# Kernel tuning notes

Measured on AMD Instinct MI355X. Metric: run time of the kernel, lower is better.

## Reference

```python
import jax, jax.numpy as jnp
import numpy as np

N_NODES = 50000


def gcn_conv(x, W, b, src, dst, n_nodes):
    # GCNConv (PyG defaults): h = x @ W; symmetric normalization with self-loops;
    # out[i] = sum_{(j->i) in E} d_j^-1/2 d_i^-1/2 h[j] + d_i^-1 h[i] + b
    h = x @ W
    ones = jnp.ones(src.shape[0], dtype=x.dtype)
    deg = jax.ops.segment_sum(ones, dst, num_segments=n_nodes) + 1.0  # +1 self-loop
    dinv = jax.lax.rsqrt(deg)
    norm = dinv[src] * dinv[dst]                       # [E]
    msg = h[src] * norm[:, None]                        # [E, D] gather
    agg = jax.ops.segment_sum(msg, dst, num_segments=n_nodes)  # scatter-add
    agg = agg + h * (dinv * dinv)[:, None]              # self-loop term
    return agg + b


def setup_inputs() -> dict:
    key = jax.random.key(0)
    k = jax.random.split(key, 8)
    in_dim, hid, out_dim = 128, 128, 64
    x = jax.random.normal(k[0], (N_NODES, in_dim), dtype=jnp.float32)
    edge_index = jax.random.randint(k[1], (2, 600000), 0, N_NODES, dtype=jnp.int64)
    s = 1.0 / np.sqrt(in_dim)
    W1 = jax.random.uniform(k[2], (in_dim, hid), jnp.float32, -s, s)
    b1 = jnp.zeros((hid,), jnp.float32)
    W2 = jax.random.uniform(k[3], (hid, hid), jnp.float32, -s, s)
    b2 = jnp.zeros((hid,), jnp.float32)
    W3 = jax.random.uniform(k[4], (hid, out_dim), jnp.float32, -s, s)
    b3 = jnp.zeros((out_dim,), jnp.float32)
    return {"x": x, "W1": W1, "b1": b1, "W2": W2, "b2": b2,
            "W3": W3, "b3": b3, "edge_index": edge_index}


def reference(x, W1, b1, W2, b2, W3, b3, edge_index):
    src, dst = edge_index[0], edge_index[1]
    n = x.shape[0]
    h = gcn_conv(x, W1, b1, src, dst, n)
    h = jax.nn.relu(h)  # dropout: inference-mode identity
    h = gcn_conv(h, W2, b2, src, dst, n)
    h = jax.nn.relu(h)
    h = gcn_conv(h, W3, b3, src, dst, n)
    return jax.nn.log_softmax(h, axis=-1)
```

## Files before the change

kernel.cpp:

```cpp
#include <hip/hip_runtime.h>
#include <math.h>

#define N_IN  128
#define N_HID 128
#define N_OUT 64

typedef _Float16 f16x8 __attribute__((ext_vector_type(8)));
typedef _Float16 f16x4 __attribute__((ext_vector_type(4)));
typedef float f32x4 __attribute__((ext_vector_type(4)));

__global__ void k_zero_int(int* __restrict__ p, int n) {
  int i = blockIdx.x * blockDim.x + threadIdx.x;
  if (i < n) p[i] = 0;
}

__global__ void k_hist(const int* __restrict__ dst, int E, int* __restrict__ cnt) {
  int i0 = (blockIdx.x * blockDim.x + threadIdx.x) * 4;
  int stride = gridDim.x * blockDim.x * 4;
  for (; i0 + 4 <= E; i0 += stride) {
    int4 d = *reinterpret_cast<const int4*>(&dst[i0]);
    atomicAdd(&cnt[d.x], 1);
    atomicAdd(&cnt[d.y], 1);
    atomicAdd(&cnt[d.z], 1);
    atomicAdd(&cnt[d.w], 1);
  }
  if (i0 < E)
    for (; i0 < E; ++i0) atomicAdd(&cnt[dst[i0]], 1);
}

#define SCAN_CHUNK 512

__global__ __launch_bounds__(SCAN_CHUNK) void k_block_sums(
    const int* __restrict__ cnt, int n, int* __restrict__ bsum) {
  __shared__ int s[SCAN_CHUNK];
  int i = blockIdx.x * SCAN_CHUNK + threadIdx.x;
  s[threadIdx.x] = (i < n) ? cnt[i] : 0;
  __syncthreads();
  for (int off = SCAN_CHUNK / 2; off > 0; off >>= 1) {
    if (threadIdx.x < off) s[threadIdx.x] += s[threadIdx.x + off];
    __syncthreads();
  }
  if (threadIdx.x == 0) bsum[blockIdx.x] = s[0];
}

__global__ __launch_bounds__(128) void k_scan_bsums(int* __restrict__ bsum, int nb) {
  __shared__ int s[128];
  int t = threadIdx.x;
  if (nb <= 128) {
    int v = (t < nb) ? bsum[t] : 0;
    s[t] = v;
    __syncthreads();
    for (int off = 1; off < 128; off <<= 1) {
      int u = (t >= off) ? s[t - off] : 0;
      __syncthreads();
      s[t] += u;
      __syncthreads();
    }
    if (t < nb) bsum[t] = s[t] - v;
  } else if (t == 0) {
    int acc = 0;
    for (int i = 0; i < nb; ++i) { int v = bsum[i]; bsum[i] = acc; acc += v; }
  }
}

__global__ __launch_bounds__(SCAN_CHUNK) void k_scan_final(
    const int* __restrict__ cnt, int n, const int* __restrict__ bsum,
    int* __restrict__ rowptr, float* __restrict__ dinv, int E) {
  __shared__ int s[SCAN_CHUNK];
  int i = blockIdx.x * SCAN_CHUNK + threadIdx.x;
  int v = (i < n) ? cnt[i] : 0;
  s[threadIdx.x] = v;
  __syncthreads();
  for (int off = 1; off < SCAN_CHUNK; off <<= 1) {
    int t = (threadIdx.x >= off) ? s[threadIdx.x - off] : 0;
    __syncthreads();
    s[threadIdx.x] += t;
    __syncthreads();
  }
  if (i < n) {
    rowptr[i] = bsum[blockIdx.x] + s[threadIdx.x] - v;
    dinv[i] = rsqrtf((float)v + 1.0f);
    if (i == n - 1) rowptr[n] = E;
  }
}

__global__ void k_fill(const int* __restrict__ src, const int* __restrict__ dst, int E,
                       const int* __restrict__ rowptr, int* __restrict__ cnt,
                       int* __restrict__ csr) {
  int i0 = (blockIdx.x * blockDim.x + threadIdx.x) * 4;
  int stride = gridDim.x * blockDim.x * 4;
  for (; i0 + 4 <= E; i0 += stride) {
    int4 d = *reinterpret_cast<const int4*>(&dst[i0]);
    int4 sr = *reinterpret_cast<const int4*>(&src[i0]);
    csr[rowptr[d.x] + atomicSub(&cnt[d.x], 1) - 1] = sr.x;
    csr[rowptr[d.y] + atomicSub(&cnt[d.y], 1) - 1] = sr.y;
    csr[rowptr[d.z] + atomicSub(&cnt[d.z], 1) - 1] = sr.z;
    csr[rowptr[d.w] + atomicSub(&cnt[d.w], 1) - 1] = sr.w;
  }
  if (i0 < E)
    for (; i0 < E; ++i0) {
      int d = dst[i0];
      csr[rowptr[d] + atomicSub(&cnt[d], 1) - 1] = src[i0];
    }
}

__device__ inline void pack_one(const float* __restrict__ W, _Float16* __restrict__ Wp,
                                int N, int K, int idx) {
  int l = idx & 63;
  int ts = idx >> 6;
  int KS = K / 32;
  int t = ts / KS, s = ts - t * KS;
  int col = t * 16 + (l & 15);
  int k0 = s * 32 + (l >> 4) * 8;
  f16x8 f;
#pragma unroll
  for (int j = 0; j < 8; ++j) f[j] = (_Float16)W[(size_t)(k0 + j) * N + col];
  *reinterpret_cast<f16x8*>(&Wp[(size_t)idx * 8]) = f;
}

__global__ void k_pack_all(const float* __restrict__ W1, const float* __restrict__ W2,
                           const float* __restrict__ W3, _Float16* __restrict__ Wp1,
                           _Float16* __restrict__ Wp2, _Float16* __restrict__ Wp3) {
  int idx = blockIdx.x * blockDim.x + threadIdx.x;
  if (idx < 2048) pack_one(W1, Wp1, N_HID, N_IN, idx);
  else if (idx < 4096) pack_one(W2, Wp2, N_HID, N_HID, idx - 2048);
  else if (idx < 5120) pack_one(W3, Wp3, N_OUT, N_HID, idx - 4096);
}

__global__ __launch_bounds__(256) void k_gemm1(
    const float* __restrict__ A, const _Float16* __restrict__ Wp,
    const float* __restrict__ dinv, _Float16* __restrict__ out, int M) {
  constexpr int N = N_HID, K = 128, KS = K / 32, NT = N / 16;
  int lane = threadIdx.x & 63;
  int wave = threadIdx.x >> 6;
  int rowbase = blockIdx.x * 64 + wave * 16;
  int arow = rowbase + (lane & 15);
  int arc = arow < M ? arow : M - 1;
  int k0 = (lane >> 4) * 8;

  f16x8 afrag[KS];
#pragma unroll
  for (int s = 0; s < KS; ++s) {
    float4 v0 = *reinterpret_cast<const float4*>(&A[(size_t)arc * K + s * 32 + k0]);
    float4 v1 = *reinterpret_cast<const float4*>(&A[(size_t)arc * K + s * 32 + k0 + 4]);
    f16x8 f;
    f[0] = (_Float16)v0.x; f[1] = (_Float16)v0.y;
    f[2] = (_Float16)v0.z; f[3] = (_Float16)v0.w;
    f[4] = (_Float16)v1.x; f[5] = (_Float16)v1.y;
    f[6] = (_Float16)v1.z; f[7] = (_Float16)v1.w;
    afrag[s] = f;
  }

  f32x4 acc[NT] = {};
#pragma unroll
  for (int t = 0; t < NT; ++t)
#pragma unroll
    for (int s = 0; s < KS; ++s) {
      f16x8 b = *reinterpret_cast<const f16x8*>(&Wp[((size_t)(t * KS + s) * 64 + lane) * 8]);
      acc[t] = __builtin_amdgcn_mfma_f32_16x16x32_f16(afrag[s], b, acc[t], 0, 0, 0);
    }

  int crow = (lane >> 4) * 4;
  int col = lane & 15;
#pragma unroll
  for (int r = 0; r < 4; ++r) {
    int grow = rowbase + crow + r;
    if (grow < M) {
      float dv = dinv[grow];
#pragma unroll
      for (int t = 0; t < NT; ++t)
        out[(size_t)grow * N + t * 16 + col] = (_Float16)(acc[t][r] * dv);
    }
  }
}

template <int NOUT>
__global__ __launch_bounds__(256) void k_agg_gemm(
    const _Float16* __restrict__ hs, const float* __restrict__ dinv,
    const int* __restrict__ rowptr, const int* __restrict__ csr,
    const float* __restrict__ bias, const _Float16* __restrict__ Wp,
    _Float16* __restrict__ out, int n, int E) {
  constexpr int D = 128, KS = 4, NT = NOUT / 16, TPW = NT / 4;
  __shared__ __align__(16) _Float16 sm[16][D + 8];
  int lane = threadIdx.x & 63, wave = threadIdx.x >> 6;
  int h = lane >> 5;
  int j = lane & 31;
  int nodebase = blockIdx.x * 16;
  int nA = nodebase + wave * 4 + 2 * h;
  int nB = nA + 1;
  int cA = min(nA, n - 1), cB = min(nB, n - 1);
  float wsA = nA < n ? 1.f : 0.f, wsB = nB < n ? 1.f : 0.f;
  int begA = rowptr[cA], endA = nA < n ? rowptr[cA + 1] : begA;
  int begB = rowptr[cB], endB = nB < n ? rowptr[cB + 1] : begB;

  float accA[4], accB[4];
  {
    f16x4 sA = *reinterpret_cast<const f16x4*>(&hs[(size_t)cA * D + 4 * j]);
    f16x4 sB = *reinterpret_cast<const f16x4*>(&hs[(size_t)cB * D + 4 * j]);
#pragma unroll
    for (int k = 0; k < 4; ++k) {
      accA[k] = wsA * (float)sA[k];
      accB[k] = wsB * (float)sB[k];
    }
  }

  int eA = begA, eB = begB;
  while (eA < endA || eB < endB) {
    int ia[4], ib[4];
    float wa[4], wb[4];
#pragma unroll
    for (int u = 0; u < 4; ++u) {
      int pA = eA + u, pB = eB + u;
      wa[u] = pA < endA ? 1.f : 0.f;
      wb[u] = pB < endB ? 1.f : 0.f;
      ia[u] = csr[min(pA, E - 1)];
      ib[u] = csr[min(pB, E - 1)];
    }
    f16x4 va[4], vb[4];
#pragma unroll
    for (int u = 0; u < 4; ++u) {
      va[u] = *reinterpret_cast<const f16x4*>(&hs[(size_t)ia[u] * D + 4 * j]);
      vb[u] = *reinterpret_cast<const f16x4*>(&hs[(size_t)ib[u] * D + 4 * j]);
    }
#pragma unroll
    for (int u = 0; u < 4; ++u)
#pragma unroll
      for (int k = 0; k < 4; ++k) {
        accA[k] = fmaf(wa[u], (float)va[u][k], accA[k]);
        accB[k] = fmaf(wb[u], (float)vb[u][k], accB[k]);
      }
    eA += 4; eB += 4;
  }

  {
    float4 bv = *reinterpret_cast<const float4*>(&bias[4 * j]);
    const float* bp = reinterpret_cast<const float*>(&bv);
    float dvA = dinv[cA], dvB = dinv[cB];
    f16x4 pA, pB;
#pragma unroll
    for (int k = 0; k < 4; ++k) {
      pA[k] = (_Float16)fmaxf(dvA * accA[k] + bp[k], 0.f);
      pB[k] = (_Float16)fmaxf(dvB * accB[k] + bp[k], 0.f);
    }
    int lr = wave * 4 + 2 * h;
    *reinterpret_cast<f16x4*>(&sm[lr][4 * j]) = pA;
    *reinterpret_cast<f16x4*>(&sm[lr + 1][4 * j]) = pB;
  }
  __syncthreads();

  int r = lane & 15, k0 = (lane >> 4) * 8;
  f16x8 af[KS];
#pragma unroll
  for (int s = 0; s < KS; ++s)
    af[s] = *reinterpret_cast<const f16x8*>(&sm[r][s * 32 + k0]);

  f32x4 acc[TPW] = {};
#pragma unroll
  for (int tt = 0; tt < TPW; ++tt) {
    int t = wave * TPW + tt;
#pragma unroll
    for (int s = 0; s < KS; ++s) {
      f16x8 b = *reinterpret_cast<const f16x8*>(&Wp[((size_t)(t * KS + s) * 64 + lane) * 8]);
      acc[tt] = __builtin_amdgcn_mfma_f32_16x16x32_f16(af[s], b, acc[tt], 0, 0, 0);
    }
  }

  int crow = (lane >> 4) * 4, col = lane & 15;
#pragma unroll
  for (int r4 = 0; r4 < 4; ++r4) {
    int node = nodebase + crow + r4;
    if (node < n) {
      float dv = dinv[node];
#pragma unroll
      for (int tt = 0; tt < TPW; ++tt)
        out[(size_t)node * NOUT + (wave * TPW + tt) * 16 + col] =
            (_Float16)(acc[tt][r4] * dv);
    }
  }
}

__global__ __launch_bounds__(256) void k_agg64_lsm(
    const _Float16* __restrict__ hs, const float* __restrict__ dinv,
    const int* __restrict__ rowptr, const int* __restrict__ csr,
    const float* __restrict__ bias, float* __restrict__ out, int n, int E) {
  constexpr int D = 64;
  int lane = threadIdx.x & 63, wave = threadIdx.x >> 6;
  int q = lane >> 4, j = lane & 15;
  int node = blockIdx.x * 16 + wave * 4 + q;
  int c = min(node, n - 1);
  float ws = node < n ? 1.f : 0.f;
  int beg = rowptr[c], end = node < n ? rowptr[c + 1] : beg;

  float acc[4];
  {
    f16x4 sv = *reinterpret_cast<const f16x4*>(&hs[(size_t)c * D + 4 * j]);
#pragma unroll
    for (int k = 0; k < 4; ++k) acc[k] = ws * (float)sv[k];
  }

  for (int e = beg; e < end; e += 4) {
    int ii[4];
    float ww[4];
#pragma unroll
    for (int u = 0; u < 4; ++u) {
      int p = e + u;
      ww[u] = p < end ? 1.f : 0.f;
      ii[u] = csr[min(p, E - 1)];
    }
    f16x4 vv[4];
#pragma unroll
    for (int u = 0; u < 4; ++u)
      vv[u] = *reinterpret_cast<const f16x4*>(&hs[(size_t)ii[u] * D + 4 * j]);
#pragma unroll
    for (int u = 0; u < 4; ++u)
#pragma unroll
      for (int k = 0; k < 4; ++k) acc[k] = fmaf(ww[u], (float)vv[u][k], acc[k]);
  }

  float dv = dinv[c];
  float val[4];
#pragma unroll
  for (int k = 0; k < 4; ++k) val[k] = dv * acc[k] + bias[4 * j + k];

  float m = fmaxf(fmaxf(val[0], val[1]), fmaxf(val[2], val[3]));
#pragma unroll
  for (int o = 8; o > 0; o >>= 1) m = fmaxf(m, __shfl_xor(m, o));
  float ss = 0.f;
#pragma unroll
  for (int k = 0; k < 4; ++k) ss += expf(val[k] - m);
#pragma unroll
  for (int o = 8; o > 0; o >>= 1) ss += __shfl_xor(ss, o);
  float lse = m + logf(ss);

  if (node < n) {
    float4 o4 = make_float4(val[0] - lse, val[1] - lse, val[2] - lse, val[3] - lse);
    *reinterpret_cast<float4*>(&out[(size_t)node * D + 4 * j]) = o4;
  }
}

extern "C" void kernel_launch(void* const* d_in, const int* in_sizes, int n_in,
                              void* d_out, int out_size, void* d_ws, size_t ws_size,
                              hipStream_t stream) {
  const float* x  = (const float*)d_in[0];
  const float* W1 = (const float*)d_in[1];
  const float* b1 = (const float*)d_in[2];
  const float* W2 = (const float*)d_in[3];
  const float* b2 = (const float*)d_in[4];
  const float* W3 = (const float*)d_in[5];
  const float* b3 = (const float*)d_in[6];
  const int*   ei = (const int*)d_in[7];

  int n = in_sizes[0] / N_IN;
  int E = in_sizes[7] / 2;
  const int* src = ei;
  const int* dst = ei + E;

  char* w = (char*)d_ws;
  size_t off = 0;
  auto alloc = [&](size_t bytes) -> void* {
    void* p = w + off;
    off = (off + bytes + 255) & ~(size_t)255;
    return p;
  };
  _Float16* hs1 = (_Float16*)alloc((size_t)n * N_HID * sizeof(_Float16));
  _Float16* hs2 = (_Float16*)alloc((size_t)n * N_HID * sizeof(_Float16));
  _Float16* hs3 = (_Float16*)alloc((size_t)n * N_OUT * sizeof(_Float16));
  _Float16* Wp1 = (_Float16*)alloc((size_t)N_IN * N_HID * sizeof(_Float16));
  _Float16* Wp2 = (_Float16*)alloc((size_t)N_HID * N_HID * sizeof(_Float16));
  _Float16* Wp3 = (_Float16*)alloc((size_t)N_HID * N_OUT * sizeof(_Float16));
  float* dinv = (float*)alloc((size_t)n * sizeof(float));
  int* cnt = (int*)alloc((size_t)n * sizeof(int));
  int* rowptr = (int*)alloc((size_t)(n + 1) * sizeof(int));
  int* csr = (int*)alloc((size_t)E * sizeof(int));
  int* bsum = (int*)alloc(4096);

  k_zero_int<<<(n + 255) / 256, 256, 0, stream>>>(cnt, n);
  {
    int blocks = min((E / 4 + 255) / 256, 1024);
    k_hist<<<blocks, 256, 0, stream>>>(dst, E, cnt);
    int nb = (n + SCAN_CHUNK - 1) / SCAN_CHUNK;
    k_block_sums<<<nb, SCAN_CHUNK, 0, stream>>>(cnt, n, bsum);
    k_scan_bsums<<<1, 128, 0, stream>>>(bsum, nb);
    k_scan_final<<<nb, SCAN_CHUNK, 0, stream>>>(cnt, n, bsum, rowptr, dinv, E);
    k_fill<<<blocks, 256, 0, stream>>>(src, dst, E, rowptr, cnt, csr);
  }

  k_pack_all<<<20, 256, 0, stream>>>(W1, W2, W3, Wp1, Wp2, Wp3);

  int gb = (n + 63) / 64;
  int ab = (n + 15) / 16;
  k_gemm1<<<gb, 256, 0, stream>>>(x, Wp1, dinv, hs1, n);
  k_agg_gemm<N_HID><<<ab, 256, 0, stream>>>(hs1, dinv, rowptr, csr, b1, Wp2, hs2, n, E);
  k_agg_gemm<N_OUT><<<ab, 256, 0, stream>>>(hs2, dinv, rowptr, csr, b2, Wp3, hs3, n, E);
  k_agg64_lsm<<<ab, 256, 0, stream>>>(hs3, dinv, rowptr, csr, b3, (float*)d_out, n, E);
}
```

Before: 166.6 us.

## Stage CSR indices in LDS, widen agg tiles, fuse scan with weight packing

The separate zeroing, three-kernel scan and pack kernels are replaced by a memset and a single kernel in which block 0 does a serial-chunk 1024-thread scan and the remaining blocks pack weights. The aggregation kernels now handle 32 nodes per block, stage the block's contiguous CSR index range in shared memory, and have each half-wave gather several nodes at once, with two MFMA row tiles reusing each weight fragment. The aim is fewer launches, less redundant index traffic and more memory-level parallelism in the gather. In exchange, block 0 does the whole scan alone and there are fewer aggregation blocks with more registers per thread.

```diff
diff --git a/kernel.cpp b/kernel.cpp
--- a/kernel.cpp
+++ b/kernel.cpp
@@ -8,11 +8,6 @@
 typedef _Float16 f16x8 __attribute__((ext_vector_type(8)));
 typedef _Float16 f16x4 __attribute__((ext_vector_type(4)));
 typedef float f32x4 __attribute__((ext_vector_type(4)));
-
-__global__ void k_zero_int(int* __restrict__ p, int n) {
-  int i = blockIdx.x * blockDim.x + threadIdx.x;
-  if (i < n) p[i] = 0;
-}
 
 __global__ void k_hist(const int* __restrict__ dst, int E, int* __restrict__ cnt) {
   int i0 = (blockIdx.x * blockDim.x + threadIdx.x) * 4;
@@ -28,60 +23,62 @@
     for (; i0 < E; ++i0) atomicAdd(&cnt[dst[i0]], 1);
 }
 
-#define SCAN_CHUNK 512
-
-__global__ __launch_bounds__(SCAN_CHUNK) void k_block_sums(
-    const int* __restrict__ cnt, int n, int* __restrict__ bsum) {
-  __shared__ int s[SCAN_CHUNK];
-  int i = blockIdx.x * SCAN_CHUNK + threadIdx.x;
-  s[threadIdx.x] = (i < n) ? cnt[i] : 0;
+__device__ inline void pack_one(const float* __restrict__ W, _Float16* __restrict__ Wp,
+                                int N, int K, int idx) {
+  int l = idx & 63;
+  int ts = idx >> 6;
+  int KS = K / 32;
+  int t = ts / KS, s = ts - t * KS;
+  int col = t * 16 + (l & 15);
+  int k0 = s * 32 + (l >> 4) * 8;
+  f16x8 f;
+#pragma unroll
+  for (int j = 0; j < 8; ++j) f[j] = (_Float16)W[(size_t)(k0 + j) * N + col];
+  *reinterpret_cast<f16x8*>(&Wp[(size_t)idx * 8]) = f;
+}
+
+#define SCAN_THREADS 1024
+__global__ __launch_bounds__(SCAN_THREADS) void k_scan_pack(
+    const int* __restrict__ cnt, int n, int E,
+    int* __restrict__ rowptr, float* __restrict__ dinv,
+    const float* __restrict__ W1, const float* __restrict__ W2,
+    const float* __restrict__ W3, _Float16* __restrict__ Wp1,
+    _Float16* __restrict__ Wp2, _Float16* __restrict__ Wp3) {
+  if (blockIdx.x > 0) {
+    int idx = (int)(blockIdx.x - 1) * SCAN_THREADS + threadIdx.x;
+    if (idx < 2048) pack_one(W1, Wp1, N_HID, N_IN, idx);
+    else if (idx < 4096) pack_one(W2, Wp2, N_HID, N_HID, idx - 2048);
+    else if (idx < 5120) pack_one(W3, Wp3, N_OUT, N_HID, idx - 4096);
+    return;
+  }
+  __shared__ int ssum[SCAN_THREADS];
+  int t = threadIdx.x;
+  int C = (n + SCAN_THREADS - 1) / SCAN_THREADS;
+  int base = t * C;
+  int lsum = 0;
+  for (int i = 0; i < C; ++i) {
+    int ii = base + i;
+    if (ii < n) lsum += cnt[ii];
+  }
+  ssum[t] = lsum;
   __syncthreads();
-  for (int off = SCAN_CHUNK / 2; off > 0; off >>= 1) {
-    if (threadIdx.x < off) s[threadIdx.x] += s[threadIdx.x + off];
+  for (int off = 1; off < SCAN_THREADS; off <<= 1) {
+    int u = (t >= off) ? ssum[t - off] : 0;
     __syncthreads();
-  }
-  if (threadIdx.x == 0) bsum[blockIdx.x] = s[0];
-}
-
-__global__ __launch_bounds__(128) void k_scan_bsums(int* __restrict__ bsum, int nb) {
-  __shared__ int s[128];
-  int t = threadIdx.x;
-  if (nb <= 128) {
-    int v = (t < nb) ? bsum[t] : 0;
-    s[t] = v;
+    ssum[t] += u;
     __syncthreads();
-    for (int off = 1; off < 128; off <<= 1) {
-      int u = (t >= off) ? s[t - off] : 0;
-      __syncthreads();
-      s[t] += u;
-      __syncthreads();
-    }
-    if (t < nb) bsum[t] = s[t] - v;
-  } else if (t == 0) {
-    int acc = 0;
-    for (int i = 0; i < nb; ++i) { int v = bsum[i]; bsum[i] = acc; acc += v; }
-  }
-}
-
-__global__ __launch_bounds__(SCAN_CHUNK) void k_scan_final(
-    const int* __restrict__ cnt, int n, const int* __restrict__ bsum,
-    int* __restrict__ rowptr, float* __restrict__ dinv, int E) {
-  __shared__ int s[SCAN_CHUNK];
-  int i = blockIdx.x * SCAN_CHUNK + threadIdx.x;
-  int v = (i < n) ? cnt[i] : 0;
-  s[threadIdx.x] = v;
-  __syncthreads();
-  for (int off = 1; off < SCAN_CHUNK; off <<= 1) {
-    int t = (threadIdx.x >= off) ? s[threadIdx.x - off] : 0;
-    __syncthreads();
-    s[threadIdx.x] += t;
-    __syncthreads();
-  }
-  if (i < n) {
-    rowptr[i] = bsum[blockIdx.x] + s[threadIdx.x] - v;
-    dinv[i] = rsqrtf((float)v + 1.0f);
-    if (i == n - 1) rowptr[n] = E;
-  }
+  }
+  int pref = ssum[t] - lsum;
+  for (int i = 0; i < C; ++i) {
+    int ii = base + i;
+    if (ii < n) {
+      int v = cnt[ii];
+      rowptr[ii] = pref;
+      dinv[ii] = rsqrtf((float)v + 1.0f);
+      pref += v;
+    }
+  }
+  if (t == 0) rowptr[n] = E;
 }
 
 __global__ void k_fill(const int* __restrict__ src, const int* __restrict__ dst, int E,
@@ -104,29 +101,6 @@
     }
 }
 
-__device__ inline void pack_one(const float* __restrict__ W, _Float16* __restrict__ Wp,
-                                int N, int K, int idx) {
-  int l = idx & 63;
-  int ts = idx >> 6;
-  int KS = K / 32;
-  int t = ts / KS, s = ts - t * KS;
-  int col = t * 16 + (l & 15);
-  int k0 = s * 32 + (l >> 4) * 8;
-  f16x8 f;
-#pragma unroll
-  for (int j = 0; j < 8; ++j) f[j] = (_Float16)W[(size_t)(k0 + j) * N + col];
-  *reinterpret_cast<f16x8*>(&Wp[(size_t)idx * 8]) = f;
-}
-
-__global__ void k_pack_all(const float* __restrict__ W1, const float* __restrict__ W2,
-                           const float* __restrict__ W3, _Float16* __restrict__ Wp1,
-                           _Float16* __restrict__ Wp2, _Float16* __restrict__ Wp3) {
-  int idx = blockIdx.x * blockDim.x + threadIdx.x;
-  if (idx < 2048) pack_one(W1, Wp1, N_HID, N_IN, idx);
-  else if (idx < 4096) pack_one(W2, Wp2, N_HID, N_HID, idx - 2048);
-  else if (idx < 5120) pack_one(W3, Wp3, N_OUT, N_HID, idx - 4096);
-}
-
 __global__ __launch_bounds__(256) void k_gemm1(
     const float* __restrict__ A, const _Float16* __restrict__ Wp,
     const float* __restrict__ dinv, _Float16* __restrict__ out, int M) {
@@ -174,167 +148,235 @@
   }
 }
 
+#define MAXE 1536
 template <int NOUT>
 __global__ __launch_bounds__(256) void k_agg_gemm(
     const _Float16* __restrict__ hs, const float* __restrict__ dinv,
     const int* __restrict__ rowptr, const int* __restrict__ csr,
     const float* __restrict__ bias, const _Float16* __restrict__ Wp,
-    _Float16* __restrict__ out, int n, int E) {
-  constexpr int D = 128, KS = 4, NT = NOUT / 16, TPW = NT / 4;
-  __shared__ __align__(16) _Float16 sm[16][D + 8];
-  int lane = threadIdx.x & 63, wave = threadIdx.x >> 6;
+    _Float16* __restrict__ out, int n) {
+  constexpr int D = 128, KS = 4, NT = NOUT / 16, TPW = NT / 4, BM = 32;
+  __shared__ int sh_idx[MAXE];
+  __shared__ __align__(16) _Float16 sm[BM][D + 8];
+  int tid = threadIdx.x;
+  int lane = tid & 63, wave = tid >> 6;
+  int nodebase = blockIdx.x * BM;
+  int nEnd = min(nodebase + BM, n);
+  int blockBeg = rowptr[nodebase];
+  int blockEnd = rowptr[nEnd];
+  int total = blockEnd - blockBeg;
+  int staged = min(total, MAXE);
+  for (int i = tid; i < staged; i += 256) sh_idx[i] = csr[blockBeg + i];
+  __syncthreads();
+
   int h = lane >> 5;
   int j = lane & 31;
-  int nodebase = blockIdx.x * 16;
-  int nA = nodebase + wave * 4 + 2 * h;
-  int nB = nA + 1;
-  int cA = min(nA, n - 1), cB = min(nB, n - 1);
-  float wsA = nA < n ? 1.f : 0.f, wsB = nB < n ? 1.f : 0.f;
-  int begA = rowptr[cA], endA = nA < n ? rowptr[cA + 1] : begA;
-  int begB = rowptr[cB], endB = nB < n ? rowptr[cB + 1] : begB;
-
-  float accA[4], accB[4];
-  {
-    f16x4 sA = *reinterpret_cast<const f16x4*>(&hs[(size_t)cA * D + 4 * j]);
-    f16x4 sB = *reinterpret_cast<const f16x4*>(&hs[(size_t)cB * D + 4 * j]);
-#pragma unroll
-    for (int k = 0; k < 4; ++k) {
-      accA[k] = wsA * (float)sA[k];
-      accB[k] = wsB * (float)sB[k];
-    }
-  }
-
-  int eA = begA, eB = begB;
-  while (eA < endA || eB < endB) {
-    int ia[4], ib[4];
-    float wa[4], wb[4];
-#pragma unroll
-    for (int u = 0; u < 4; ++u) {
-      int pA = eA + u, pB = eB + u;
-      wa[u] = pA < endA ? 1.f : 0.f;
-      wb[u] = pB < endB ? 1.f : 0.f;
-      ia[u] = csr[min(pA, E - 1)];
-      ib[u] = csr[min(pB, E - 1)];
-    }
-    f16x4 va[4], vb[4];
-#pragma unroll
-    for (int u = 0; u < 4; ++u) {
-      va[u] = *reinterpret_cast<const f16x4*>(&hs[(size_t)ia[u] * D + 4 * j]);
-      vb[u] = *reinterpret_cast<const f16x4*>(&hs[(size_t)ib[u] * D + 4 * j]);
-    }
-#pragma unroll
-    for (int u = 0; u < 4; ++u)
-#pragma unroll
-      for (int k = 0; k < 4; ++k) {
-        accA[k] = fmaf(wa[u], (float)va[u][k], accA[k]);
-        accB[k] = fmaf(wb[u], (float)vb[u][k], accB[k]);
+  int g = wave * 2 + h;
+
+  float acc[4][4];
+  int e[4], endL[4];
+#pragma unroll
+  for (int c = 0; c < 4; ++c) {
+    int node = nodebase + g * 4 + c;
+    int cn = min(node, n - 1);
+    bool valid = node < n;
+    e[c] = rowptr[cn] - blockBeg;
+    endL[c] = valid ? rowptr[cn + 1] - blockBeg : e[c];
+    f16x4 sv = *reinterpret_cast<const f16x4*>(&hs[(size_t)cn * D + 4 * j]);
+#pragma unroll
+    for (int k = 0; k < 4; ++k) acc[c][k] = valid ? (float)sv[k] : 0.f;
+  }
+
+  auto gather = [&](auto getidx) {
+    for (;;) {
+      bool active = false;
+#pragma unroll
+      for (int c = 0; c < 4; ++c) active |= (e[c] < endL[c]);
+      if (!active) break;
+      float ww[4][2];
+      int id[4][2];
+#pragma unroll
+      for (int c = 0; c < 4; ++c)
+#pragma unroll
+        for (int u = 0; u < 2; ++u) {
+          int p = e[c] + u;
+          ww[c][u] = (p < endL[c]) ? 1.f : 0.f;
+          id[c][u] = getidx(min(p, total - 1));
+        }
+      f16x4 vv[4][2];
+#pragma unroll
+      for (int c = 0; c < 4; ++c)
+#pragma unroll
+        for (int u = 0; u < 2; ++u)
+          vv[c][u] = *reinterpret_cast<const f16x4*>(&hs[(size_t)id[c][u] * D + 4 * j]);
+#pragma unroll
+      for (int c = 0; c < 4; ++c) {
+#pragma unroll
+        for (int u = 0; u < 2; ++u)
+#pragma unroll
+          for (int k = 0; k < 4; ++k)
+            acc[c][k] = fmaf(ww[c][u], (float)vv[c][u][k], acc[c][k]);
+        e[c] += 2;
       }
-    eA += 4; eB += 4;
+    }
+  };
+  if (total > 0) {
+    if (total <= MAXE)
+      gather([&](int p) { return sh_idx[p]; });
+    else
+      gather([&](int p) { return csr[blockBeg + p]; });
   }
 
   {
     float4 bv = *reinterpret_cast<const float4*>(&bias[4 * j]);
     const float* bp = reinterpret_cast<const float*>(&bv);
-    float dvA = dinv[cA], dvB = dinv[cB];
-    f16x4 pA, pB;
-#pragma unroll
-    for (int k = 0; k < 4; ++k) {
-      pA[k] = (_Float16)fmaxf(dvA * accA[k] + bp[k], 0.f);
-      pB[k] = (_Float16)fmaxf(dvB * accB[k] + bp[k], 0.f);
-    }
-    int lr = wave * 4 + 2 * h;
-    *reinterpret_cast<f16x4*>(&sm[lr][4 * j]) = pA;
-    *reinterpret_cast<f16x4*>(&sm[lr + 1][4 * j]) = pB;
+#pragma unroll
+    for (int c = 0; c < 4; ++c) {
+      int node = nodebase + g * 4 + c;
+      float dv = dinv[min(node, n - 1)];
+      f16x4 pv;
+#pragma unroll
+      for (int k = 0; k < 4; ++k) pv[k] = (_Float16)fmaxf(dv * acc[c][k] + bp[k], 0.f);
+      *reinterpret_cast<f16x4*>(&sm[g * 4 + c][4 * j]) = pv;
+    }
   }
   __syncthreads();
 
   int r = lane & 15, k0 = (lane >> 4) * 8;
-  f16x8 af[KS];
-#pragma unroll
-  for (int s = 0; s < KS; ++s)
-    af[s] = *reinterpret_cast<const f16x8*>(&sm[r][s * 32 + k0]);
-
-  f32x4 acc[TPW] = {};
-#pragma unroll
-  for (int tt = 0; tt < TPW; ++tt) {
-    int t = wave * TPW + tt;
+  f16x8 af[2][KS];
+#pragma unroll
+  for (int rt = 0; rt < 2; ++rt)
+#pragma unroll
+    for (int s = 0; s < KS; ++s)
+      af[rt][s] = *reinterpret_cast<const f16x8*>(&sm[rt * 16 + r][s * 32 + k0]);
+
+  f32x4 acc2[TPW][2] = {};
+#pragma unroll
+  for (int ct = 0; ct < TPW; ++ct) {
+    int t = wave * TPW + ct;
 #pragma unroll
     for (int s = 0; s < KS; ++s) {
       f16x8 b = *reinterpret_cast<const f16x8*>(&Wp[((size_t)(t * KS + s) * 64 + lane) * 8]);
-      acc[tt] = __builtin_amdgcn_mfma_f32_16x16x32_f16(af[s], b, acc[tt], 0, 0, 0);
+#pragma unroll
+      for (int rt = 0; rt < 2; ++rt)
+        acc2[ct][rt] = __builtin_amdgcn_mfma_f32_16x16x32_f16(af[rt][s], b, acc2[ct][rt], 0, 0, 0);
     }
   }
 
   int crow = (lane >> 4) * 4, col = lane & 15;
 #pragma unroll
-  for (int r4 = 0; r4 < 4; ++r4) {
-    int node = nodebase + crow + r4;
-    if (node < n) {
-      float dv = dinv[node];
-#pragma unroll
-      for (int tt = 0; tt < TPW; ++tt)
-        out[(size_t)node * NOUT + (wave * TPW + tt) * 16 + col] =
-            (_Float16)(acc[tt][r4] * dv);
-    }
-  }
+  for (int rt = 0; rt < 2; ++rt)
+#pragma unroll
+    for (int r4 = 0; r4 < 4; ++r4) {
+      int node = nodebase + rt * 16 + crow + r4;
+      if (node < n) {
+        float dv = dinv[node];
+#pragma unroll
+        for (int ct = 0; ct < TPW; ++ct)
+          out[(size_t)node * NOUT + (wave * TPW + ct) * 16 + col] =
+              (_Float16)(acc2[ct][rt][r4] * dv);
+      }
+    }
 }
 
 __global__ __launch_bounds__(256) void k_agg64_lsm(
     const _Float16* __restrict__ hs, const float* __restrict__ dinv,
     const int* __restrict__ rowptr, const int* __restrict__ csr,
-    const float* __restrict__ bias, float* __restrict__ out, int n, int E) {
-  constexpr int D = 64;
-  int lane = threadIdx.x & 63, wave = threadIdx.x >> 6;
-  int q = lane >> 4, j = lane & 15;
-  int node = blockIdx.x * 16 + wave * 4 + q;
-  int c = min(node, n - 1);
-  float ws = node < n ? 1.f : 0.f;
-  int beg = rowptr[c], end = node < n ? rowptr[c + 1] : beg;
-
-  float acc[4];
-  {
-    f16x4 sv = *reinterpret_cast<const f16x4*>(&hs[(size_t)c * D + 4 * j]);
-#pragma unroll
-    for (int k = 0; k < 4; ++k) acc[k] = ws * (float)sv[k];
-  }
-
-  for (int e = beg; e < end; e += 4) {
-    int ii[4];
-    float ww[4];
-#pragma unroll
-    for (int u = 0; u < 4; ++u) {
-      int p = e + u;
-      ww[u] = p < end ? 1.f : 0.f;
-      ii[u] = csr[min(p, E - 1)];
-    }
-    f16x4 vv[4];
-#pragma unroll
-    for (int u = 0; u < 4; ++u)
-      vv[u] = *reinterpret_cast<const f16x4*>(&hs[(size_t)ii[u] * D + 4 * j]);
-#pragma unroll
-    for (int u = 0; u < 4; ++u)
-#pragma unroll
-      for (int k = 0; k < 4; ++k) acc[k] = fmaf(ww[u], (float)vv[u][k], acc[k]);
-  }
-
-  float dv = dinv[c];
-  float val[4];
-#pragma unroll
-  for (int k = 0; k < 4; ++k) val[k] = dv * acc[k] + bias[4 * j + k];
-
-  float m = fmaxf(fmaxf(val[0], val[1]), fmaxf(val[2], val[3]));
-#pragma unroll
-  for (int o = 8; o > 0; o >>= 1) m = fmaxf(m, __shfl_xor(m, o));
-  float ss = 0.f;
-#pragma unroll
-  for (int k = 0; k < 4; ++k) ss += expf(val[k] - m);
-#pragma unroll
-  for (int o = 8; o > 0; o >>= 1) ss += __shfl_xor(ss, o);
-  float lse = m + logf(ss);
-
-  if (node < n) {
-    float4 o4 = make_float4(val[0] - lse, val[1] - lse, val[2] - lse, val[3] - lse);
-    *reinterpret_cast<float4*>(&out[(size_t)node * D + 4 * j]) = o4;
+    const float* __restrict__ bias, float* __restrict__ out, int n) {
+  constexpr int D = 64, BM = 32;
+  __shared__ int sh_idx[MAXE];
+  int tid = threadIdx.x;
+  int lane = tid & 63, wave = tid >> 6;
+  int nodebase = blockIdx.x * BM;
+  int nEnd = min(nodebase + BM, n);
+  int blockBeg = rowptr[nodebase];
+  int blockEnd = rowptr[nEnd];
+  int total = blockEnd - blockBeg;
+  int staged = min(total, MAXE);
+  for (int i = tid; i < staged; i += 256) sh_idx[i] = csr[blockBeg + i];
+  __syncthreads();
+
+  int q = lane >> 4;
+  int j = lane & 15;
+  int g = wave * 4 + q;
+
+  float acc[2][4];
+  int e[2], endL[2];
+#pragma unroll
+  for (int c = 0; c < 2; ++c) {
+    int node = nodebase + g * 2 + c;
+    int cn = min(node, n - 1);
+    bool valid = node < n;
+    e[c] = rowptr[cn] - blockBeg;
+    endL[c] = valid ? rowptr[cn + 1] - blockBeg : e[c];
+    f16x4 sv = *reinterpret_cast<const f16x4*>(&hs[(size_t)cn * D + 4 * j]);
+#pragma unroll
+    for (int k = 0; k < 4; ++k) acc[c][k] = valid ? (float)sv[k] : 0.f;
+  }
+
+  auto gather = [&](auto getidx) {
+    for (;;) {
+      bool active = false;
+#pragma unroll
+      for (int c = 0; c < 2; ++c) active |= (e[c] < endL[c]);
+      if (!active) break;
+      float ww[2][4];
+      int id[2][4];
+#pragma unroll
+      for (int c = 0; c < 2; ++c)
+#pragma unroll
+        for (int u = 0; u < 4; ++u) {
+          int p = e[c] + u;
+          ww[c][u] = (p < endL[c]) ? 1.f : 0.f;
+          id[c][u] = getidx(min(p, total - 1));
+        }
+      f16x4 vv[2][4];
+#pragma unroll
+      for (int c = 0; c < 2; ++c)
+#pragma unroll
+        for (int u = 0; u < 4; ++u)
+          vv[c][u] = *reinterpret_cast<const f16x4*>(&hs[(size_t)id[c][u] * D + 4 * j]);
+#pragma unroll
+      for (int c = 0; c < 2; ++c) {
+#pragma unroll
+        for (int u = 0; u < 4; ++u)
+#pragma unroll
+          for (int k = 0; k < 4; ++k)
+            acc[c][k] = fmaf(ww[c][u], (float)vv[c][u][k], acc[c][k]);
+        e[c] += 4;
+      }
+    }
+  };
+  if (total > 0) {
+    if (total <= MAXE)
+      gather([&](int p) { return sh_idx[p]; });
+    else
+      gather([&](int p) { return csr[blockBeg + p]; });
+  }
+
+#pragma unroll
+  for (int c = 0; c < 2; ++c) {
+    int node = nodebase + g * 2 + c;
+    int cn = min(node, n - 1);
+    float dv = dinv[cn];
+    float val[4];
+#pragma unroll
+    for (int k = 0; k < 4; ++k) val[k] = dv * acc[c][k] + bias[4 * j + k];
+
+    float m = fmaxf(fmaxf(val[0], val[1]), fmaxf(val[2], val[3]));
+#pragma unroll
+    for (int o = 8; o > 0; o >>= 1) m = fmaxf(m, __shfl_xor(m, o));
+    float ss = 0.f;
+#pragma unroll
+    for (int k = 0; k < 4; ++k) ss += expf(val[k] - m);
+#pragma unroll
+    for (int o = 8; o > 0; o >>= 1) ss += __shfl_xor(ss, o);
+    float lse = m + logf(ss);
+
+    if (node < n) {
+      float4 o4 = make_float4(val[0] - lse, val[1] - lse, val[2] - lse, val[3] - lse);
+      *reinterpret_cast<float4*>(&out[(size_t)node * D + 4 * j]) = o4;
+    }
   }
 }
 
@@ -372,25 +414,18 @@
   int* cnt = (int*)alloc((size_t)n * sizeof(int));
   int* rowptr = (int*)alloc((size_t)(n + 1) * sizeof(int));
   int* csr = (int*)alloc((size_t)E * sizeof(int));
-  int* bsum = (int*)alloc(4096);
-
-  k_zero_int<<<(n + 255) / 256, 256, 0, stream>>>(cnt, n);
-  {
-    int blocks = min((E / 4 + 255) / 256, 1024);
-    k_hist<<<blocks, 256, 0, stream>>>(dst, E, cnt);
-    int nb = (n + SCAN_CHUNK - 1) / SCAN_CHUNK;
-    k_block_sums<<<nb, SCAN_CHUNK, 0, stream>>>(cnt, n, bsum);
-    k_scan_bsums<<<1, 128, 0, stream>>>(bsum, nb);
-    k_scan_final<<<nb, SCAN_CHUNK, 0, stream>>>(cnt, n, bsum, rowptr, dinv, E);
-    k_fill<<<blocks, 256, 0, stream>>>(src, dst, E, rowptr, cnt, csr);
-  }
-
-  k_pack_all<<<20, 256, 0, stream>>>(W1, W2, W3, Wp1, Wp2, Wp3);
+
+  hipMemsetAsync(cnt, 0, (size_t)n * sizeof(int), stream);
+  int blocks = min((E / 4 + 255) / 256, 1024);
+  k_hist<<<blocks, 256, 0, stream>>>(dst, E, cnt);
+  k_scan_pack<<<6, SCAN_THREADS, 0, stream>>>(cnt, n, E, rowptr, dinv,
+                                              W1, W2, W3, Wp1, Wp2, Wp3);
+  k_fill<<<blocks, 256, 0, stream>>>(src, dst, E, rowptr, cnt, csr);
 
   int gb = (n + 63) / 64;
-  int ab = (n + 15) / 16;
+  int ab = (n + 31) / 32;
   k_gemm1<<<gb, 256, 0, stream>>>(x, Wp1, dinv, hs1, n);
-  k_agg_gemm<N_HID><<<ab, 256, 0, stream>>>(hs1, dinv, rowptr, csr, b1, Wp2, hs2, n, E);
-  k_agg_gemm<N_OUT><<<ab, 256, 0, stream>>>(hs2, dinv, rowptr, csr, b2, Wp3, hs3, n, E);
-  k_agg64_lsm<<<ab, 256, 0, stream>>>(hs3, dinv, rowptr, csr, b3, (float*)d_out, n, E);
-}
+  k_agg_gemm<N_HID><<<ab, 256, 0, stream>>>(hs1, dinv, rowptr, csr, b1, Wp2, hs2, n);
+  k_agg_gemm<N_OUT><<<ab, 256, 0, stream>>>(hs2, dinv, rowptr, csr, b2, Wp3, hs3, n);
+  k_agg64_lsm<<<ab, 256, 0, stream>>>(hs3, dinv, rowptr, csr, b3, (float*)d_out, n);
+}
```

New measurement: 289.5 us. 73.8% more time.

## Fuse CSR-build launches and software-pipeline edge index loads in aggregation

Applied to the files above, without the earlier changes.

Replaces the zero kernel with a memset and merges the three-kernel scan into one kernel where each block recomputes its prefix by summing all earlier counts. Weight packing is folded into the CSR fill kernel as extra blocks. The aggregation loops in both aggregation kernels now prefetch the next four CSR indices before accumulating the current ones, to hide index-load latency. Together these cut launch count and gather latency, at the cost of redundant prefix reads in later scan blocks and more registers.

```diff
diff --git a/kernel.cpp b/kernel.cpp
--- a/kernel.cpp
+++ b/kernel.cpp
@@ -8,11 +8,6 @@
 typedef _Float16 f16x8 __attribute__((ext_vector_type(8)));
 typedef _Float16 f16x4 __attribute__((ext_vector_type(4)));
 typedef float f32x4 __attribute__((ext_vector_type(4)));
-
-__global__ void k_zero_int(int* __restrict__ p, int n) {
-  int i = blockIdx.x * blockDim.x + threadIdx.x;
-  if (i < n) p[i] = 0;
-}
 
 __global__ void k_hist(const int* __restrict__ dst, int E, int* __restrict__ cnt) {
   int i0 = (blockIdx.x * blockDim.x + threadIdx.x) * 4;
@@ -28,80 +23,38 @@
     for (; i0 < E; ++i0) atomicAdd(&cnt[dst[i0]], 1);
 }
 
-#define SCAN_CHUNK 512
-
-__global__ __launch_bounds__(SCAN_CHUNK) void k_block_sums(
-    const int* __restrict__ cnt, int n, int* __restrict__ bsum) {
-  __shared__ int s[SCAN_CHUNK];
-  int i = blockIdx.x * SCAN_CHUNK + threadIdx.x;
-  s[threadIdx.x] = (i < n) ? cnt[i] : 0;
+#define SCHUNK 512
+__global__ __launch_bounds__(SCHUNK) void k_scan_all(
+    const int* __restrict__ cnt, int n, int E,
+    int* __restrict__ rowptr, float* __restrict__ dinv) {
+  __shared__ int sh[SCHUNK];
+  int t = threadIdx.x;
+  int base = blockIdx.x * SCHUNK;
+  int pre = 0;
+  for (int i = t; i < base; i += SCHUNK) pre += cnt[i];
+  sh[t] = pre;
   __syncthreads();
-  for (int off = SCAN_CHUNK / 2; off > 0; off >>= 1) {
-    if (threadIdx.x < off) s[threadIdx.x] += s[threadIdx.x + off];
+  for (int o = SCHUNK / 2; o > 0; o >>= 1) {
+    if (t < o) sh[t] += sh[t + o];
     __syncthreads();
   }
-  if (threadIdx.x == 0) bsum[blockIdx.x] = s[0];
-}
-
-__global__ __launch_bounds__(128) void k_scan_bsums(int* __restrict__ bsum, int nb) {
-  __shared__ int s[128];
-  int t = threadIdx.x;
-  if (nb <= 128) {
-    int v = (t < nb) ? bsum[t] : 0;
-    s[t] = v;
+  int blockpre = sh[0];
+  __syncthreads();
+  int v = (base + t < n) ? cnt[base + t] : 0;
+  sh[t] = v;
+  __syncthreads();
+  for (int o = 1; o < SCHUNK; o <<= 1) {
+    int u = (t >= o) ? sh[t - o] : 0;
     __syncthreads();
-    for (int off = 1; off < 128; off <<= 1) {
-      int u = (t >= off) ? s[t - off] : 0;
-      __syncthreads();
-      s[t] += u;
-      __syncthreads();
-    }
-    if (t < nb) bsum[t] = s[t] - v;
-  } else if (t == 0) {
-    int acc = 0;
-    for (int i = 0; i < nb; ++i) { int v = bsum[i]; bsum[i] = acc; acc += v; }
-  }
-}
-
-__global__ __launch_bounds__(SCAN_CHUNK) void k_scan_final(
-    const int* __restrict__ cnt, int n, const int* __restrict__ bsum,
-    int* __restrict__ rowptr, float* __restrict__ dinv, int E) {
-  __shared__ int s[SCAN_CHUNK];
-  int i = blockIdx.x * SCAN_CHUNK + threadIdx.x;
-  int v = (i < n) ? cnt[i] : 0;
-  s[threadIdx.x] = v;
-  __syncthreads();
-  for (int off = 1; off < SCAN_CHUNK; off <<= 1) {
-    int t = (threadIdx.x >= off) ? s[threadIdx.x - off] : 0;
+    sh[t] += u;
     __syncthreads();
-    s[threadIdx.x] += t;
-    __syncthreads();
-  }
+  }
+  int i = base + t;
   if (i < n) {
-    rowptr[i] = bsum[blockIdx.x] + s[threadIdx.x] - v;
+    rowptr[i] = blockpre + sh[t] - v;
     dinv[i] = rsqrtf((float)v + 1.0f);
     if (i == n - 1) rowptr[n] = E;
   }
-}
-
-__global__ void k_fill(const int* __restrict__ src, const int* __restrict__ dst, int E,
-                       const int* __restrict__ rowptr, int* __restrict__ cnt,
-                       int* __restrict__ csr) {
-  int i0 = (blockIdx.x * blockDim.x + threadIdx.x) * 4;
-  int stride = gridDim.x * blockDim.x * 4;
-  for (; i0 + 4 <= E; i0 += stride) {
-    int4 d = *reinterpret_cast<const int4*>(&dst[i0]);
-    int4 sr = *reinterpret_cast<const int4*>(&src[i0]);
-    csr[rowptr[d.x] + atomicSub(&cnt[d.x], 1) - 1] = sr.x;
-    csr[rowptr[d.y] + atomicSub(&cnt[d.y], 1) - 1] = sr.y;
-    csr[rowptr[d.z] + atomicSub(&cnt[d.z], 1) - 1] = sr.z;
-    csr[rowptr[d.w] + atomicSub(&cnt[d.w], 1) - 1] = sr.w;
-  }
-  if (i0 < E)
-    for (; i0 < E; ++i0) {
-      int d = dst[i0];
-      csr[rowptr[d] + atomicSub(&cnt[d], 1) - 1] = src[i0];
-    }
 }
 
 __device__ inline void pack_one(const float* __restrict__ W, _Float16* __restrict__ Wp,
@@ -118,13 +71,34 @@
   *reinterpret_cast<f16x8*>(&Wp[(size_t)idx * 8]) = f;
 }
 
-__global__ void k_pack_all(const float* __restrict__ W1, const float* __restrict__ W2,
-                           const float* __restrict__ W3, _Float16* __restrict__ Wp1,
-                           _Float16* __restrict__ Wp2, _Float16* __restrict__ Wp3) {
-  int idx = blockIdx.x * blockDim.x + threadIdx.x;
-  if (idx < 2048) pack_one(W1, Wp1, N_HID, N_IN, idx);
-  else if (idx < 4096) pack_one(W2, Wp2, N_HID, N_HID, idx - 2048);
-  else if (idx < 5120) pack_one(W3, Wp3, N_OUT, N_HID, idx - 4096);
+__global__ void k_fill_pack(const int* __restrict__ src, const int* __restrict__ dst,
+                            int E, const int* __restrict__ rowptr, int* __restrict__ cnt,
+                            int* __restrict__ csr, int fb,
+                            const float* __restrict__ W1, const float* __restrict__ W2,
+                            const float* __restrict__ W3, _Float16* __restrict__ Wp1,
+                            _Float16* __restrict__ Wp2, _Float16* __restrict__ Wp3) {
+  if (blockIdx.x >= fb) {
+    int idx = (int)(blockIdx.x - fb) * 256 + threadIdx.x;
+    if (idx < 2048) pack_one(W1, Wp1, N_HID, N_IN, idx);
+    else if (idx < 4096) pack_one(W2, Wp2, N_HID, N_HID, idx - 2048);
+    else if (idx < 5120) pack_one(W3, Wp3, N_OUT, N_HID, idx - 4096);
+    return;
+  }
+  int i0 = (blockIdx.x * 256 + threadIdx.x) * 4;
+  int stride = fb * 256 * 4;
+  for (; i0 + 4 <= E; i0 += stride) {
+    int4 d = *reinterpret_cast<const int4*>(&dst[i0]);
+    int4 sr = *reinterpret_cast<const int4*>(&src[i0]);
+    csr[rowptr[d.x] + atomicSub(&cnt[d.x], 1) - 1] = sr.x;
+    csr[rowptr[d.y] + atomicSub(&cnt[d.y], 1) - 1] = sr.y;
+    csr[rowptr[d.z] + atomicSub(&cnt[d.z], 1) - 1] = sr.z;
+    csr[rowptr[d.w] + atomicSub(&cnt[d.w], 1) - 1] = sr.w;
+  }
+  if (i0 < E && threadIdx.x == 0 && blockIdx.x == 0)
+    for (int i = (E >> 2) << 2; i < E; ++i) {
+      int d = dst[i];
+      csr[rowptr[d] + atomicSub(&cnt[d], 1) - 1] = src[i];
+    }
 }
 
 __global__ __launch_bounds__(256) void k_gemm1(
@@ -205,23 +179,32 @@
   }
 
   int eA = begA, eB = begB;
-  while (eA < endA || eB < endB) {
-    int ia[4], ib[4];
-    float wa[4], wb[4];
+  int ia[4], ib[4];
+  float wa[4], wb[4];
+  auto loadIdx = [&](int a0, int b0, int* iax, int* ibx, float* wax, float* wbx) {
 #pragma unroll
     for (int u = 0; u < 4; ++u) {
-      int pA = eA + u, pB = eB + u;
-      wa[u] = pA < endA ? 1.f : 0.f;
-      wb[u] = pB < endB ? 1.f : 0.f;
-      ia[u] = csr[min(pA, E - 1)];
-      ib[u] = csr[min(pB, E - 1)];
-    }
+      int pA = a0 + u, pB = b0 + u;
+      wax[u] = pA < endA ? 1.f : 0.f;
+      wbx[u] = pB < endB ? 1.f : 0.f;
+      iax[u] = csr[min(pA, E - 1)];
+      ibx[u] = csr[min(pB, E - 1)];
+    }
+  };
+  bool any = (eA < endA) || (eB < endB);
+  if (any) loadIdx(eA, eB, ia, ib, wa, wb);
+  while (any) {
     f16x4 va[4], vb[4];
 #pragma unroll
     for (int u = 0; u < 4; ++u) {
       va[u] = *reinterpret_cast<const f16x4*>(&hs[(size_t)ia[u] * D + 4 * j]);
       vb[u] = *reinterpret_cast<const f16x4*>(&hs[(size_t)ib[u] * D + 4 * j]);
     }
+    int eA2 = eA + 4, eB2 = eB + 4;
+    bool any2 = (eA2 < endA) || (eB2 < endB);
+    int ia2[4], ib2[4];
+    float wa2[4], wb2[4];
+    if (any2) loadIdx(eA2, eB2, ia2, ib2, wa2, wb2);
 #pragma unroll
     for (int u = 0; u < 4; ++u)
 #pragma unroll
@@ -229,7 +212,12 @@
         accA[k] = fmaf(wa[u], (float)va[u][k], accA[k]);
         accB[k] = fmaf(wb[u], (float)vb[u][k], accB[k]);
       }
-    eA += 4; eB += 4;
+    eA = eA2; eB = eB2; any = any2;
+#pragma unroll
+    for (int u = 0; u < 4; ++u) {
+      ia[u] = ia2[u]; ib[u] = ib2[u];
+      wa[u] = wa2[u]; wb[u] = wb2[u];
+    }
   }
 
   {
@@ -298,23 +286,36 @@
     for (int k = 0; k < 4; ++k) acc[k] = ws * (float)sv[k];
   }
 
-  for (int e = beg; e < end; e += 4) {
-    int ii[4];
-    float ww[4];
+  int e = beg;
+  int ii[4];
+  float ww[4];
+  auto loadIdx = [&](int e0, int* iix, float* wwx) {
 #pragma unroll
     for (int u = 0; u < 4; ++u) {
-      int p = e + u;
-      ww[u] = p < end ? 1.f : 0.f;
-      ii[u] = csr[min(p, E - 1)];
-    }
+      int p = e0 + u;
+      wwx[u] = p < end ? 1.f : 0.f;
+      iix[u] = csr[min(p, E - 1)];
+    }
+  };
+  bool any = e < end;
+  if (any) loadIdx(e, ii, ww);
+  while (any) {
     f16x4 vv[4];
 #pragma unroll
     for (int u = 0; u < 4; ++u)
       vv[u] = *reinterpret_cast<const f16x4*>(&hs[(size_t)ii[u] * D + 4 * j]);
+    int e2 = e + 4;
+    bool any2 = e2 < end;
+    int ii2[4];
+    float ww2[4];
+    if (any2) loadIdx(e2, ii2, ww2);
 #pragma unroll
     for (int u = 0; u < 4; ++u)
 #pragma unroll
       for (int k = 0; k < 4; ++k) acc[k] = fmaf(ww[u], (float)vv[u][k], acc[k]);
+    e = e2; any = any2;
+#pragma unroll
+    for (int u = 0; u < 4; ++u) { ii[u] = ii2[u]; ww[u] = ww2[u]; }
   }
 
   float dv = dinv[c];
@@ -372,20 +373,14 @@
   int* cnt = (int*)alloc((size_t)n * sizeof(int));
   int* rowptr = (int*)alloc((size_t)(n + 1) * sizeof(int));
   int* csr = (int*)alloc((size_t)E * sizeof(int));
-  int* bsum = (int*)alloc(4096);
-
-  k_zero_int<<<(n + 255) / 256, 256, 0, stream>>>(cnt, n);
-  {
-    int blocks = min((E / 4 + 255) / 256, 1024);
-    k_hist<<<blocks, 256, 0, stream>>>(dst, E, cnt);
-    int nb = (n + SCAN_CHUNK - 1) / SCAN_CHUNK;
-    k_block_sums<<<nb, SCAN_CHUNK, 0, stream>>>(cnt, n, bsum);
-    k_scan_bsums<<<1, 128, 0, stream>>>(bsum, nb);
-    k_scan_final<<<nb, SCAN_CHUNK, 0, stream>>>(cnt, n, bsum, rowptr, dinv, E);
-    k_fill<<<blocks, 256, 0, stream>>>(src, dst, E, rowptr, cnt, csr);
-  }
-
-  k_pack_all<<<20, 256, 0, stream>>>(W1, W2, W3, Wp1, Wp2, Wp3);
+
+  hipMemsetAsync(cnt, 0, (size_t)n * sizeof(int), stream);
+  int fb = min((E / 4 + 255) / 256, 1024);
+  k_hist<<<fb, 256, 0, stream>>>(dst, E, cnt);
+  int nb = (n + SCHUNK - 1) / SCHUNK;
+  k_scan_all<<<nb, SCHUNK, 0, stream>>>(cnt, n, E, rowptr, dinv);
+  k_fill_pack<<<fb + 20, 256, 0, stream>>>(src, dst, E, rowptr, cnt, csr, fb,
+                                           W1, W2, W3, Wp1, Wp2, Wp3);
 
   int gb = (n + 63) / 64;
   int ab = (n + 15) / 16;
```

After: 176.1 us. 1.06x slower.
